# Optimization experiments

Hardware: AMD Instinct MI355X
Metric: run time of the kernel (lower is better)

Reference implementation:

```python
import jax, jax.numpy as jnp
import numpy as np

IMAGE_W, IMAGE_H = 1024, 800
STRIDES = (8, 16, 32, 64, 128)
LEVEL_HW = ((100, 128), (50, 64), (25, 32), (13, 16), (7, 8))
TOP_N = 1000
MIN_SCORE = 0.01
NMS_THR = 0.6
MAX_DET = 100
NUM_CLASSES = 80
BATCH = 16


def _grid(h, w, stride, b):
    ys = (jnp.arange(h, dtype=jnp.float32) + 0.5) * stride
    xs = (jnp.arange(w, dtype=jnp.float32) + 0.5) * stride
    gx, gy = jnp.meshgrid(xs, ys)  # [h, w]
    pos = jnp.stack([gx, gy], axis=-1)  # [h, w, 2] = (x, y)
    return jnp.broadcast_to(pos, (b, h, w, 2))


def setup_inputs() -> dict:
    key = jax.random.key(0)
    inp = {}
    for i, ((h, w), s) in enumerate(zip(LEVEL_HW, STRIDES)):
        key, k1, k2, k3 = jax.random.split(key, 4)
        inp[f"cls{i}"] = jax.random.normal(k1, (BATCH, h, w, NUM_CLASSES), jnp.float32)
        # +3 so exp(reg) gives realistic ~20px box extents
        inp[f"reg{i}"] = jax.random.normal(k2, (BATCH, h, w, 4), jnp.float32) + 3.0
        inp[f"ctr{i}"] = jax.random.normal(k3, (BATCH, h, w, 1), jnp.float32)
        inp[f"pos{i}"] = _grid(h, w, s, BATCH)
    return inp


def _level_filter(cls, reg, ctr, pos):
    b = cls.shape[0]
    cls = jax.nn.sigmoid(cls).reshape(b, -1, NUM_CLASSES)
    reg = jnp.exp(reg).reshape(b, -1, 4)
    ctr = jax.nn.sigmoid(ctr).reshape(b, -1)
    pos = pos.reshape(b, -1, 2)
    scores = jnp.sqrt(jnp.max(cls, axis=2) * ctr)  # [b, n]
    classes = jnp.argmax(cls, axis=2)  # [b, n] int
    if scores.shape[1] >= TOP_N:
        scores, idx = jax.lax.top_k(scores, TOP_N)
        classes = jnp.take_along_axis(classes, idx, axis=1)
        reg = jnp.take_along_axis(reg, idx[..., None], axis=1)
        pos = jnp.take_along_axis(pos, idx[..., None], axis=1)
        cls = jnp.take_along_axis(cls, idx[..., None], axis=1)
    return scores, classes, reg, pos, cls


def _decode_boxes(reg, pos):
    # ltrb offsets -> x1y1x2y2, truncate to int (torch .int()), clamp to image
    xy_min = pos - reg[..., 0:2]
    xy_max = pos + reg[..., 2:4]
    bx = jnp.trunc(jnp.concatenate([xy_min, xy_max], axis=-1))
    x1 = jnp.maximum(bx[..., 0], 0.0)
    y1 = jnp.maximum(bx[..., 1], 0.0)
    x2 = jnp.minimum(bx[..., 2], IMAGE_W - 1.0)
    y2 = jnp.minimum(bx[..., 3], IMAGE_H - 1.0)
    return jnp.stack([x1, y1, x2, y2], axis=-1)


def _nms_image(scores, classes, boxes, clsp):
    valid = scores > MIN_SCORE
    order = jnp.argsort(jnp.where(valid, -scores, jnp.inf))  # valid, desc score first
    s = scores[order]
    c = classes[order].astype(jnp.float32)
    b = boxes[order]
    cp = clsp[order]
    v = valid[order]
    # pairwise IoU (keep/suppress decisions are not differentiated)
    bb = jax.lax.stop_gradient(b)
    area = (bb[:, 2] - bb[:, 0]) * (bb[:, 3] - bb[:, 1])
    lt = jnp.maximum(bb[:, None, :2], bb[None, :, :2])
    rb = jnp.minimum(bb[:, None, 2:], bb[None, :, 2:])
    wh = jnp.maximum(rb - lt, 0.0)
    inter = wh[..., 0] * wh[..., 1]
    iou = inter / (area[:, None] + area[None, :] - inter)
    n = s.shape[0]
    idxs = jnp.arange(n)

    def body(i, keep):
        sup = keep[i] & (iou[i] > NMS_THR) & (idxs > i)
        return keep & ~sup

    keep = jax.lax.fori_loop(0, n, body, v)
    rank = jnp.cumsum(keep) - 1
    slot = jnp.where(keep & (rank < MAX_DET), rank, MAX_DET)  # MAX_DET -> dropped
    out_s = jnp.full((MAX_DET,), -1.0, jnp.float32).at[slot].set(s, mode="drop")
    out_c = jnp.full((MAX_DET,), -1.0, jnp.float32).at[slot].set(c, mode="drop")
    out_b = jnp.full((MAX_DET, 4), -1.0, jnp.float32).at[slot].set(b, mode="drop")
    out_cp = jnp.full((MAX_DET, NUM_CLASSES), -1.0, jnp.float32).at[slot].set(cp, mode="drop")
    return out_s, out_c, out_b, out_cp


def reference(cls0, cls1, cls2, cls3, cls4, reg0, reg1, reg2, reg3, reg4,
              ctr0, ctr1, ctr2, ctr3, ctr4, pos0, pos1, pos2, pos3, pos4):
    clss = [cls0, cls1, cls2, cls3, cls4]
    regs = [reg0, reg1, reg2, reg3, reg4]
    ctrs = [ctr0, ctr1, ctr2, ctr3, ctr4]
    poss = [pos0, pos1, pos2, pos3, pos4]
    parts = [_level_filter(c, r, t, p) for c, r, t, p in zip(clss, regs, ctrs, poss)]
    scores = jnp.concatenate([p[0] for p in parts], axis=1)
    classes = jnp.concatenate([p[1] for p in parts], axis=1)
    reg = jnp.concatenate([p[2] for p in parts], axis=1)
    pos = jnp.concatenate([p[3] for p in parts], axis=1)
    clsp = jnp.concatenate([p[4] for p in parts], axis=1)
    boxes = _decode_boxes(reg, pos)
    return jax.vmap(_nms_image)(scores, classes, boxes, clsp)
```

## Files before the change

### kernel.cpp

```cpp
#include <hip/hip_runtime.h>
#include <math.h>

#define TOTAL_G 17064
#define BATCHN  16
#define ALLF    0xFFFFFFFFFFFFFFFFull
#define INVALID_HI 0xC3DC28F5u

typedef unsigned long long u64;
typedef unsigned int u32;
typedef unsigned short u16;

#define KEYS0_OFF   0
#define KEYS1_OFF   1638400
#define KEYS234_OFF 2048000
#define CLSI_OFF    2187264
#define NC_OFF      2733312
#define T512_OFF    2733824
#define KR_OFF      2733952
#define MSK_OFF     2799488
#define SLOTK_OFF   3323776

struct Ptrs {
  const float *cls0,*cls1,*cls2,*cls3,*cls4;
  const float *reg0,*reg1,*reg2,*reg3,*reg4;
  const float *ctr0,*ctr1,*ctr2,*ctr3,*ctr4;
  const float *pos0,*pos1,*pos2,*pos3,*pos4;
  char *ws;
};

__device__ __forceinline__ float sigd(float x) {
  return (float)(1.0 / (1.0 + exp(-(double)x)));
}
__device__ __forceinline__ float dexp(float x) {
  return (float)exp((double)x);
}
__device__ __forceinline__ void levinfo(int gid, int& lev, int& idx, int& nl) {
  if      (gid < 12800) { lev=0; idx=gid;        nl=12800; }
  else if (gid < 16000) { lev=1; idx=gid-12800;  nl=3200;  }
  else if (gid < 16800) { lev=2; idx=gid-16000;  nl=800;   }
  else if (gid < 17008) { lev=3; idx=gid-16800;  nl=208;   }
  else                  { lev=4; idx=gid-17008;  nl=56;    }
}

__device__ __forceinline__ u64* krank_of(char* ws, int b) {
  return (u64*)(ws + KR_OFF + (size_t)b * 4096);
}
__device__ __forceinline__ u64* msk_of(char* ws, int b) {
  return (u64*)(ws + MSK_OFF + (size_t)b * 32768);
}
__device__ __forceinline__ u64* slotkey_of(char* ws, int b) {
  return (u64*)(ws + SLOTK_OFF + (size_t)b * 800);
}

__device__ __forceinline__ float4 decode_box(const Ptrs& P, int b, int gid) {
  int lev, idx, nl; levinfo(gid, lev, idx, nl);
  const float *rp, *pp;
  if      (lev == 0) { rp = P.reg0; pp = P.pos0; }
  else if (lev == 1) { rp = P.reg1; pp = P.pos1; }
  else if (lev == 2) { rp = P.reg2; pp = P.pos2; }
  else if (lev == 3) { rp = P.reg3; pp = P.pos3; }
  else               { rp = P.reg4; pp = P.pos4; }
  float4 rv = *(const float4*)(rp + (size_t)(b * nl + idx) * 4);
  float2 pv = *(const float2*)(pp + (size_t)(b * nl + idx) * 2);
  float e0 = dexp(rv.x), e1 = dexp(rv.y), e2 = dexp(rv.z), e3 = dexp(rv.w);
  float x1 = truncf(pv.x - e0), y1 = truncf(pv.y - e1);
  float x2 = truncf(pv.x + e2), y2 = truncf(pv.y + e3);
  x1 = fmaxf(x1, 0.0f); y1 = fmaxf(y1, 0.0f);
  x2 = fminf(x2, 1023.0f); y2 = fminf(y2, 799.0f);
  return make_float4(x1, y1, x2, y2);
}

__global__ __launch_bounds__(256) void k_score(Ptrs P) {
  __shared__ float4 sk4[64 * 20];
  int b = blockIdx.y;
  int tid = threadIdx.x;
  int p0 = blockIdx.x * 64;

  #pragma unroll
  for (int it = 0; it < 5; ++it) {
    int t4 = it * 256 + tid;
    int g = p0 + t4 / 20;
    if (g < TOTAL_G) {
      int sub = t4 - (t4 / 20) * 20;
      int lev, idx, nl; levinfo(g, lev, idx, nl);
      const float* clsb;
      if      (lev == 0) clsb = P.cls0;
      else if (lev == 1) clsb = P.cls1;
      else if (lev == 2) clsb = P.cls2;
      else if (lev == 3) clsb = P.cls3;
      else               clsb = P.cls4;
      sk4[t4] = ((const float4*)(clsb + (size_t)(b * nl + idx) * 80))[sub];
    }
  }
  __syncthreads();

  int lp = tid >> 2, q = tid & 3;
  int g = p0 + lp;
  if (g >= TOTAL_G) return;

  const float4* my4 = &sk4[lp * 20 + q * 5];
  float m = -INFINITY, m2 = -INFINITY; int mi = 0;
  #pragma unroll
  for (int k = 0; k < 5; ++k) {
    float4 v = my4[k];
    int base = q * 20 + 4 * k;
    if (v.x > m) { m2 = m; m = v.x; mi = base+0; } else if (v.x > m2) m2 = v.x;
    if (v.y > m) { m2 = m; m = v.y; mi = base+1; } else if (v.y > m2) m2 = v.y;
    if (v.z > m) { m2 = m; m = v.z; mi = base+2; } else if (v.z > m2) m2 = v.z;
    if (v.w > m) { m2 = m; m = v.w; mi = base+3; } else if (v.w > m2) m2 = v.w;
  }
  #pragma unroll
  for (int xw = 1; xw <= 2; xw <<= 1) {
    float om  = __shfl_xor(m,  xw);
    float om2 = __shfl_xor(m2, xw);
    int   omi = __shfl_xor(mi, xw);
    bool take = (om > m) || (om == m && omi < mi);
    float lm  = take ? m : om;
    float wm2 = take ? om2 : m2;
    if (take) { m = om; mi = omi; }
    m2 = fmaxf(lm, wm2);
  }

  float thr = fminf(m - 1e-3f, 9.0f);
  float pmax; int ci;
  if (m2 >= thr) {
    float pv = -1.0f; int pi = 0x7fffffff;
    #pragma unroll 1
    for (int k = 0; k < 5; ++k) {
      float4 v = my4[k];
      float xs[4] = {v.x, v.y, v.z, v.w};
      #pragma unroll
      for (int e = 0; e < 4; ++e) {
        if (xs[e] >= thr) {
          float p = sigd(xs[e]);
          if (p > pv) { pv = p; pi = q * 20 + 4 * k + e; }
        }
      }
    }
    #pragma unroll
    for (int xw = 1; xw <= 2; xw <<= 1) {
      float ov = __shfl_xor(pv, xw);
      int   oi = __shfl_xor(pi, xw);
      if (ov > pv || (ov == pv && oi < pi)) { pv = ov; pi = oi; }
    }
    pmax = pv; ci = pi;
  } else {
    pmax = sigd(m); ci = mi;
  }

  if (q == 0) {
    int lev, idx, nl; levinfo(g, lev, idx, nl);
    const float* ctrb;
    if      (lev == 0) ctrb = P.ctr0;
    else if (lev == 1) ctrb = P.ctr1;
    else if (lev == 2) ctrb = P.ctr2;
    else if (lev == 3) ctrb = P.ctr3;
    else               ctrb = P.ctr4;
    float tc = ctrb[(size_t)b * nl + idx];
    float csig = sigd(tc);
    float prod = pmax * csig;
    float s = (float)sqrt((double)prod);
    ((u16*)(P.ws + CLSI_OFF))[(size_t)b * TOTAL_G + g] = (u16)ci;
    unsigned hi = ~__float_as_uint(s);
    u64 key = ((u64)hi << 15) | (unsigned)g;
    if      (lev == 0) ((u64*)(P.ws + KEYS0_OFF))  [(size_t)b * 12800 + idx] = key;
    else if (lev == 1) ((u64*)(P.ws + KEYS1_OFF))  [(size_t)b * 3200  + idx] = key;
    else               ((u64*)(P.ws + KEYS234_OFF))[(size_t)b * 1088  + (g - 16000)] = key;
  }
}

__device__ __forceinline__ u64 loadkey(const Ptrs& P, int b, int u) {
  if (u < 12800) return ((const u64*)(P.ws + KEYS0_OFF))  [(size_t)b * 12800 + u];
  if (u < 16000) return ((const u64*)(P.ws + KEYS1_OFF))  [(size_t)b * 3200  + (u - 12800)];
  return               ((const u64*)(P.ws + KEYS234_OFF))[(size_t)b * 1088  + (u - 16000)];
}
__device__ __forceinline__ ulonglong2 loadkey2(const Ptrs& P, int b, int u) {
  if (u < 12800) return *(const ulonglong2*)((const u64*)(P.ws + KEYS0_OFF)   + (size_t)b * 12800 + u);
  if (u < 16000) return *(const ulonglong2*)((const u64*)(P.ws + KEYS1_OFF)   + (size_t)b * 3200  + (u - 12800));
  return               *(const ulonglong2*)((const u64*)(P.ws + KEYS234_OFF) + (size_t)b * 1088  + (u - 16000));
}
__device__ __forceinline__ bool keep_pred(u64 k, int u, u64 T0, u64 T1) {
  bool valid = (u32)(k >> 15) < INVALID_HI;
  bool sel = (u < 12800) ? (k <= T0) : ((u < 16000) ? (k <= T1) : true);
  return valid && sel;
}

__global__ __launch_bounds__(1024) void k_mask(Ptrs P) {
  __shared__ union USh {
    u32 H[4][4096];
    struct { float4 sbox[512]; u64 smaskR[4096]; u16 parts[1024]; } M;
  } U;
  __shared__ u64 skey[512];
  __shared__ u16 srank[512];
  __shared__ int wbase[144];
  __shared__ int sN5;
  __shared__ u64 sBoundary;
  int qi = blockIdx.x, b = blockIdx.y;
  int tid = threadIdx.x, wid = tid >> 6, lane = tid & 63;
  int rep = wid & 3;
  char* ws = P.ws;

  ulonglong2 kk[9];
  #pragma unroll
  for (int it = 0; it < 9; ++it) kk[it] = loadkey2(P, b, it * 2048 + tid * 2);

  for (int i = tid; i < 4 * 4096; i += 1024) (&U.H[0][0])[i] = 0;
  __syncthreads();
  #pragma unroll
  for (int it = 0; it < 9; ++it) {
    int u = it * 2048 + tid * 2;
    if (u < TOTAL_G && (u32)(kk[it].x >> 15) < INVALID_HI)
      atomicAdd(&U.H[rep][(u32)(kk[it].x >> 29) & 0xFFF], 1u);
    if (u + 1 < TOTAL_G && (u32)(kk[it].y >> 15) < INVALID_HI)
      atomicAdd(&U.H[rep][(u32)(kk[it].y >> 29) & 0xFFF], 1u);
  }
  __syncthreads();
  for (int i = tid; i < 4096; i += 1024)
    U.H[0][i] = U.H[0][i] + U.H[1][i] + U.H[2][i] + U.H[3][i];
  __syncthreads();

  if (wid == 0) {
    u32 ssum = 0;
    #pragma unroll 8
    for (int i = 0; i < 64; ++i) {
      int ii = (i + lane) & 63;
      ssum += U.H[0][(lane << 6) + ii];
    }
    u32 inc = ssum;
    for (int o = 1; o < 64; o <<= 1) { u32 v = __shfl_up(inc, o); if (lane >= o) inc += v; }
    u64 ball = __ballot(inc >= 512u);
    if (!ball) {
      if (lane == 0) sBoundary = ((u64)INVALID_HI << 15);
    } else {
      int Wq = __ffsll(ball) - 1;
      u32 cumBefore = __shfl(inc - ssum, Wq);
      u32 v2 = U.H[0][(Wq << 6) + lane];
      u32 inc2 = v2;
      for (int o = 1; o < 64; o <<= 1) { u32 x = __shfl_up(inc2, o); if (lane >= o) inc2 += x; }
      u64 ball2 = __ballot(cumBefore + inc2 >= 512u);
      int l2 = __ffsll(ball2) - 1;
      if (lane == 0) {
        int d = (Wq << 6) + l2;
        sBoundary = (48ull << 41) | ((u64)d << 29);
      }
    }
  }
  __syncthreads();
  u64 Boundary = sBoundary;
  if (qi == 0 && tid == 0) ((u64*)(ws + T512_OFF))[b] = Boundary - 1;

  #pragma unroll
  for (int it = 0; it < 9; ++it) {
    int u = it * 2048 + tid * 2;
    bool k0 = (u     < TOTAL_G) && ((u32)(kk[it].x >> 15) < INVALID_HI) && (kk[it].x < Boundary);
    bool k1 = (u + 1 < TOTAL_G) && ((u32)(kk[it].y >> 15) < INVALID_HI) && (kk[it].y < Boundary);
    u64 b0 = __ballot(k0), b1 = __ballot(k1);
    if (lane == 0) wbase[it * 16 + wid] = __popcll(b0) + __popcll(b1);
  }
  __syncthreads();
  if (wid == 0) {
    int carry = 0;
    for (int base = 0; base < 144; base += 64) {
      int idx = base + lane;
      int v = (idx < 144) ? wbase[idx] : 0;
      int inc = v;
      for (int o = 1; o < 64; o <<= 1) { int x = __shfl_up(inc, o); if (lane >= o) inc += x; }
      if (idx < 144) wbase[idx] = inc - v + carry;
      carry += __shfl(inc, 63);
    }
    if (lane == 0) sN5 = carry;
  }
  __syncthreads();
  int n512 = sN5;
  if (qi == 0 && tid == 0) ((int*)(ws + NC_OFF))[16 + b] = n512;

  #pragma unroll
  for (int it = 0; it < 9; ++it) {
    int u = it * 2048 + tid * 2;
    bool k0 = (u     < TOTAL_G) && ((u32)(kk[it].x >> 15) < INVALID_HI) && (kk[it].x < Boundary);
    bool k1 = (u + 1 < TOTAL_G) && ((u32)(kk[it].y >> 15) < INVALID_HI) && (kk[it].y < Boundary);
    u64 b0 = __ballot(k0), b1 = __ballot(k1);
    u64 lm = (1ull << lane) - 1ull;
    int pos0 = wbase[it * 16 + wid] + __popcll(b0 & lm) + __popcll(b1 & lm);
    int pos1 = pos0 + (k0 ? 1 : 0);
    if (k0) skey[pos0] = kk[it].x;
    if (k1) skey[pos1] = kk[it].y;
  }
  __syncthreads();

  if (tid < 512) {
    if (tid < n512) {
      U.M.sbox[tid] = decode_box(P, b, (int)(skey[tid] & 0x7FFF));
    } else {
      skey[tid] = (ALLF - 511) + (u64)tid;
      U.M.sbox[tid] = make_float4(-1e30f, -1e30f, -1e30f, -1e30f);
    }
  }
  for (int i = tid; i < 512 * 8; i += 1024) U.M.smaskR[i] = 0ull;
  __syncthreads();

  {
    int t2 = tid & 511, half = tid >> 9;
    u64 mykey = skey[t2];
    int jb = half << 8, cnt = 0;
    #pragma unroll 4
    for (int j = jb; j < jb + 256; ++j) cnt += (skey[j] < mykey) ? 1 : 0;
    U.M.parts[tid] = (u16)cnt;
  }
  __syncthreads();
  if (tid < 512) srank[tid] = (u16)(U.M.parts[tid] + U.M.parts[tid + 512]);
  __syncthreads();

  int i = qi * 128 + (tid >> 3);
  int w = tid & 7;
  float4 bi = U.M.sbox[i];
  u64 ki = skey[i];
  int ri = srank[i];
  float ia = (bi.z - bi.x) * (bi.w - bi.y);
  #pragma unroll 8
  for (int bj = 0; bj < 64; ++bj) {
    int jj = (bj + w) & 63;
    int j = (w << 6) | jj;
    u64 kj = skey[j];
    if (ki < kj) {
      float4 bj4 = U.M.sbox[j];
      float ja  = (bj4.z - bj4.x) * (bj4.w - bj4.y);
      float ltx = fmaxf(bi.x, bj4.x), lty = fmaxf(bi.y, bj4.y);
      float rbx = fminf(bi.z, bj4.z), rby = fminf(bi.w, bj4.w);
      float wv = fmaxf(rbx - ltx, 0.0f), hv = fmaxf(rby - lty, 0.0f);
      float inter = wv * hv;
      float iou = inter / (ia + ja - inter);
      if (iou > 0.6f) {
        int rj = srank[j];
        atomicOr(&U.M.smaskR[ri * 8 + (rj >> 6)], 1ull << (rj & 63));
      }
    }
  }
  __syncthreads();

  {
    int il = tid >> 3, ww = tid & 7;
    int ig = qi * 128 + il;
    if (ig < n512) {
      int r = srank[ig];
      msk_of(ws, b)[r * 8 + ww] = U.M.smaskR[r * 8 + ww];
      if (ww == 0) krank_of(ws, b)[r] = skey[ig];
    }
  }
}

__device__ u64 select256(const u64* keys, int n, int t0, u32* hist, u64* shP, int* shT) {
  u64 Pfx = 3; int t = t0;
  const int SS[4] = {33, 21, 9, 0};
  const int WW[4] = {12, 12, 12, 9};
  for (int p = 0; p < 4; ++p) {
    int s = SS[p], wb = WW[p];
    u32 dmask = (1u << wb) - 1u;
    for (int i = threadIdx.x; i < 4096; i += 256) hist[i] = 0;
    __syncthreads();
    for (int i = threadIdx.x; i < n; i += 256) {
      u64 k = keys[i];
      if ((k >> (s + wb)) == Pfx) atomicAdd(&hist[(u32)(k >> s) & dmask], 1u);
    }
    __syncthreads();
    if (threadIdx.x < 64) {
      int lane = threadIdx.x;
      u32 ssum = 0;
      for (int i = 0; i < 64; ++i) ssum += hist[(lane << 6) + ((i + lane) & 63)];
      u32 inc = ssum;
      for (int o = 1; o < 64; o <<= 1) { u32 v = __shfl_up(inc, o); if (lane >= o) inc += v; }
      u64 ball = __ballot(inc >= (u32)t);
      int Wq = __ffsll(ball) - 1;
      u32 cumBefore = __shfl(inc - ssum, Wq);
      u32 v2 = hist[(Wq << 6) + lane];
      u32 inc2 = v2;
      for (int o = 1; o < 64; o <<= 1) { u32 x = __shfl_up(inc2, o); if (lane >= o) inc2 += x; }
      u64 ball2 = __ballot(cumBefore + inc2 >= (u32)t);
      int l2 = __ffsll(ball2) - 1;
      u32 cumB2 = __shfl(cumBefore + inc2 - v2, l2);
      if (lane == 0) { *shP = (Pfx << wb) | (u32)((Wq << 6) + l2); *shT = t - (int)cumB2; }
    }
    __syncthreads();
    Pfx = *shP; t = *shT;
    __syncthreads();
  }
  return Pfx;
}

__global__ __launch_bounds__(256) void k_reduce(Ptrs P) {
  __shared__ u64 smask[4096];
  __shared__ u32 keeplist[100];
  __shared__ int keptS;
  __shared__ u64 liveC[267];
  __shared__ union UF {
    u32 hist[4096];
    struct { u64 pk[256]; int pc[256]; float4 fkb[100]; } F;
  } UF_;
  __shared__ u64 shP; __shared__ int shT;
  __shared__ u64 bk; __shared__ int bc2;

  int b = blockIdx.x;
  int tid = threadIdx.x;
  char* ws = P.ws;
  int n512 = ((int*)(ws + NC_OFF))[16 + b];
  const u64* kr = krank_of(ws, b);

  const u64* gmask = msk_of(ws, b);
  for (int t = tid; t < 4096; t += 256) smask[t] = gmask[t];
  __syncthreads();

  if (tid < 64) {
    int lane = tid;
    u64 lw = 0;
    if (lane < 8) {
      int lo = lane << 6;
      int c = n512 - lo; if (c < 0) c = 0; if (c > 64) c = 64;
      lw = (c >= 64) ? ALLF : ((c > 0) ? ((1ull << c) - 1ull) : 0ull);
    }
    int kept = 0;
    while (kept < 100) {
      bool nz = (lane < 8) && (lw != 0ull);
      u64 bal = __ballot(nz);
      if (!bal) break;
      int W = __ffsll(bal) - 1;
      u64 wv = __shfl(lw, W);
      int bit = __ffsll(wv) - 1;
      int i = (W << 6) + bit;
      if (lane == 0) keeplist[kept] = (u32)i;
      kept++;
      if (lane == W) lw &= ~(1ull << bit);
      if (kept == 100) break;
      if (lane < 8) lw &= ~smask[i * 8 + lane];
    }
    if (lane == 0) keptS = kept;
  }
  __syncthreads();
  int kept = keptS;
  int keptW = kept;

  if (kept < 100) {
    u64 T0 = select256((const u64*)(ws + KEYS0_OFF) + (size_t)b * 12800, 12800, 1000,
                       UF_.hist, &shP, &shT);
    u64 T1 = select256((const u64*)(ws + KEYS1_OFF) + (size_t)b * 3200, 3200, 1000,
                       UF_.hist, &shP, &shT);
    u64 T512 = ((u64*)(ws + T512_OFF))[b];
    for (int w = tid; w < 267; w += 256) {
      int lo = w << 6;
      u64 m = 0;
      for (int e = 0; e < 64; ++e) {
        int u = lo + e;
        if (u < TOTAL_G) {
          u64 k = loadkey(P, b, u);
          if (keep_pred(k, u, T0, T1) && k > T512) m |= (1ull << e);
        }
      }
      liveC[w] = m;
    }
    if (tid < kept) UF_.F.fkb[tid] = decode_box(P, b, (int)(kr[keeplist[tid]] & 0x7FFF));
    __syncthreads();

    for (int k2 = 0; k2 < kept; ++k2) {
      float4 bi = UF_.F.fkb[k2];
      float ia = (bi.z - bi.x) * (bi.w - bi.y);
      for (int u = tid; u < TOTAL_G; u += 256) {
        if (!((liveC[u >> 6] >> (u & 63)) & 1ull)) continue;
        float4 bj4 = decode_box(P, b, u);
        float ja  = (bj4.z - bj4.x) * (bj4.w - bj4.y);
        float ltx = fmaxf(bi.x, bj4.x), lty = fmaxf(bi.y, bj4.y);
        float rbx = fminf(bi.z, bj4.z), rby = fminf(bi.w, bj4.w);
        float wv = fmaxf(rbx - ltx, 0.0f), hv = fmaxf(rby - lty, 0.0f);
        float inter = wv * hv;
        float iou = inter / (ia + ja - inter);
        if (iou > 0.6f) atomicAnd(&liveC[u >> 6], ~(1ull << (u & 63)));
      }
    }
    __syncthreads();

    while (kept < 100) {
      u64 mymin = ALLF; int myc = -1;
      for (int u = tid; u < TOTAL_G; u += 256) {
        if (!((liveC[u >> 6] >> (u & 63)) & 1ull)) continue;
        u64 k = loadkey(P, b, u);
        if (k < mymin) { mymin = k; myc = u; }
      }
      UF_.F.pk[tid] = mymin; UF_.F.pc[tid] = myc;
      __syncthreads();
      if (tid < 64) {
        u64 m = UF_.F.pk[tid]; int c0 = UF_.F.pc[tid];
        #pragma unroll
        for (int o = 64; o < 256; o += 64)
          if (UF_.F.pk[tid + o] < m) { m = UF_.F.pk[tid + o]; c0 = UF_.F.pc[tid + o]; }
        for (int o = 32; o > 0; o >>= 1) {
          u64 om = __shfl_down(m, o); int oc = __shfl_down(c0, o);
          if (om < m) { m = om; c0 = oc; }
        }
        if (tid == 0) { bk = m; bc2 = c0; }
      }
      __syncthreads();
      if (bk == ALLF) break;
      int cs = bc2;
      if (tid == 0) {
        slotkey_of(ws, b)[kept] = bk;
        atomicAnd(&liveC[cs >> 6], ~(1ull << (cs & 63)));
      }
      __syncthreads();
      kept++;
      if (kept == 100) break;
      float4 bi = decode_box(P, b, cs);
      float ia = (bi.z - bi.x) * (bi.w - bi.y);
      for (int u = tid; u < TOTAL_G; u += 256) {
        if (!((liveC[u >> 6] >> (u & 63)) & 1ull)) continue;
        float4 bj4 = decode_box(P, b, u);
        float ja  = (bj4.z - bj4.x) * (bj4.w - bj4.y);
        float ltx = fmaxf(bi.x, bj4.x), lty = fmaxf(bi.y, bj4.y);
        float rbx = fminf(bi.z, bj4.z), rby = fminf(bi.w, bj4.w);
        float wv = fmaxf(rbx - ltx, 0.0f), hv = fmaxf(rby - lty, 0.0f);
        float inter = wv * hv;
        float iou = inter / (ia + ja - inter);
        if (iou > 0.6f) atomicAnd(&liveC[u >> 6], ~(1ull << (u & 63)));
      }
      __syncthreads();
    }
  }

  if (tid < 100) {
    if (tid < keptW)      slotkey_of(ws, b)[tid] = kr[keeplist[tid]];
    else if (tid >= kept) slotkey_of(ws, b)[tid] = ALLF;
  }
}

__global__ __launch_bounds__(256) void k_out(Ptrs P, float* out) {
  int b = blockIdx.x, part = blockIdx.y;
  int s0 = part * 10;
  int tid = threadIdx.x;
  const u64* skl = slotkey_of(P.ws, b);

  if (tid < 10) {
    int s = s0 + tid;
    u64 key = skl[s];
    float os = -1.0f, oc = -1.0f;
    float4 bx = make_float4(-1.0f, -1.0f, -1.0f, -1.0f);
    if (key != ALLF) {
      int gid = (int)(key & 0x7FFF);
      os = __uint_as_float(~(u32)(key >> 15));
      oc = (float)((u16*)(P.ws + CLSI_OFF))[(size_t)b * TOTAL_G + gid];
      bx = decode_box(P, b, gid);
    }
    out[b * 100 + s] = os;
    out[1600 + b * 100 + s] = oc;
    *(float4*)(out + 3200 + (size_t)(b * 100 + s) * 4) = bx;
  }

  for (int t = tid; t < 800; t += 256) {
    int sl = t / 80, k = t - sl * 80;
    int s = s0 + sl;
    u64 key = skl[s];
    float val = -1.0f;
    if (key != ALLF) {
      int gid = (int)(key & 0x7FFF);
      int lev, idx, nl; levinfo(gid, lev, idx, nl);
      const float* cp;
      if      (lev == 0) cp = P.cls0;
      else if (lev == 1) cp = P.cls1;
      else if (lev == 2) cp = P.cls2;
      else if (lev == 3) cp = P.cls3;
      else               cp = P.cls4;
      val = sigd(cp[(size_t)(b * nl + idx) * 80 + k]);
    }
    out[9600 + (size_t)(b * 100 + s) * 80 + k] = val;
  }
}

extern "C" void kernel_launch(void* const* d_in, const int* in_sizes, int n_in,
                              void* d_out, int out_size, void* d_ws, size_t ws_size,
                              hipStream_t stream) {
  (void)in_sizes; (void)n_in; (void)out_size; (void)ws_size;
  Ptrs P;
  P.cls0 = (const float*)d_in[0];  P.reg0 = (const float*)d_in[1];
  P.ctr0 = (const float*)d_in[2];  P.pos0 = (const float*)d_in[3];
  P.cls1 = (const float*)d_in[4];  P.reg1 = (const float*)d_in[5];
  P.ctr1 = (const float*)d_in[6];  P.pos1 = (const float*)d_in[7];
  P.cls2 = (const float*)d_in[8];  P.reg2 = (const float*)d_in[9];
  P.ctr2 = (const float*)d_in[10]; P.pos2 = (const float*)d_in[11];
  P.cls3 = (const float*)d_in[12]; P.reg3 = (const float*)d_in[13];
  P.ctr3 = (const float*)d_in[14]; P.pos3 = (const float*)d_in[15];
  P.cls4 = (const float*)d_in[16]; P.reg4 = (const float*)d_in[17];
  P.ctr4 = (const float*)d_in[18]; P.pos4 = (const float*)d_in[19];
  P.ws = (char*)d_ws;

  k_score<<<dim3(267, 16), 256, 0, stream>>>(P);
  k_mask<<<dim3(4, 16), 1024, 0, stream>>>(P);
  k_reduce<<<16, 256, 0, stream>>>(P);
  k_out<<<dim3(16, 10), 256, 0, stream>>>(P, (float*)d_out);
}
```

Before: 91.41 us.

## Fuse mask, reduce and output kernels via last-block-done atomic counter

Merges the mask-building, greedy NMS reduction and output-writing kernels into one launch. The last of the four blocks per image, found with an atomic counter plus threadfence, runs the serial reduction and writes outputs directly, keeping slot keys and the boundary threshold in shared memory instead of the workspace. The reduction now runs with 1024 threads instead of 256. This removes two kernel launches and their global round trips, but the output writing is now done by only 16 blocks instead of 160, and the larger shared union may lower occupancy.

```diff
diff --git a/kernel.cpp b/kernel.cpp
--- a/kernel.cpp
+++ b/kernel.cpp
@@ -15,10 +15,8 @@
 #define KEYS234_OFF 2048000
 #define CLSI_OFF    2187264
 #define NC_OFF      2733312
-#define T512_OFF    2733824
 #define KR_OFF      2733952
 #define MSK_OFF     2799488
-#define SLOTK_OFF   3323776
 
 struct Ptrs {
   const float *cls0,*cls1,*cls2,*cls3,*cls4;
@@ -47,9 +45,6 @@
 }
 __device__ __forceinline__ u64* msk_of(char* ws, int b) {
   return (u64*)(ws + MSK_OFF + (size_t)b * 32768);
-}
-__device__ __forceinline__ u64* slotkey_of(char* ws, int b) {
-  return (u64*)(ws + SLOTK_OFF + (size_t)b * 800);
 }
 
 __device__ __forceinline__ float4 decode_box(const Ptrs& P, int b, int gid) {
@@ -75,6 +70,8 @@
   int b = blockIdx.y;
   int tid = threadIdx.x;
   int p0 = blockIdx.x * 64;
+
+  if (blockIdx.x == 0 && tid == 0) ((int*)(P.ws + NC_OFF))[b] = 0;
 
   #pragma unroll
   for (int it = 0; it < 5; ++it) {
@@ -185,16 +182,63 @@
   return valid && sel;
 }
 
-__global__ __launch_bounds__(1024) void k_mask(Ptrs P) {
+__device__ u64 select1024(const u64* keys, int n, int t0, u32* hist, u64* shP, int* shT) {
+  u64 Pfx = 3; int t = t0;
+  const int SS[4] = {33, 21, 9, 0};
+  const int WW[4] = {12, 12, 12, 9};
+  for (int p = 0; p < 4; ++p) {
+    int s = SS[p], wb = WW[p];
+    u32 dmask = (1u << wb) - 1u;
+    for (int i = threadIdx.x; i < 4096; i += 1024) hist[i] = 0;
+    __syncthreads();
+    for (int i = threadIdx.x; i < n; i += 1024) {
+      u64 k = keys[i];
+      if ((k >> (s + wb)) == Pfx) atomicAdd(&hist[(u32)(k >> s) & dmask], 1u);
+    }
+    __syncthreads();
+    if (threadIdx.x < 64) {
+      int lane = threadIdx.x;
+      u32 ssum = 0;
+      for (int i = 0; i < 64; ++i) ssum += hist[(lane << 6) + ((i + lane) & 63)];
+      u32 inc = ssum;
+      for (int o = 1; o < 64; o <<= 1) { u32 v = __shfl_up(inc, o); if (lane >= o) inc += v; }
+      u64 ball = __ballot(inc >= (u32)t);
+      int Wq = __ffsll(ball) - 1;
+      u32 cumBefore = __shfl(inc - ssum, Wq);
+      u32 v2 = hist[(Wq << 6) + lane];
+      u32 inc2 = v2;
+      for (int o = 1; o < 64; o <<= 1) { u32 x = __shfl_up(inc2, o); if (lane >= o) inc2 += x; }
+      u64 ball2 = __ballot(cumBefore + inc2 >= (u32)t);
+      int l2 = __ffsll(ball2) - 1;
+      u32 cumB2 = __shfl(cumBefore + inc2 - v2, l2);
+      if (lane == 0) { *shP = (Pfx << wb) | (u32)((Wq << 6) + l2); *shT = t - (int)cumB2; }
+    }
+    __syncthreads();
+    Pfx = *shP; t = *shT;
+    __syncthreads();
+  }
+  return Pfx;
+}
+
+__global__ __launch_bounds__(1024) void k_maskred(Ptrs P, float* out) {
   __shared__ union USh {
     u32 H[4][4096];
     struct { float4 sbox[512]; u64 smaskR[4096]; u16 parts[1024]; } M;
+    struct { u64 smask[4096]; u32 hist[4096]; u64 pk[1024]; int pc[1024];
+             float4 fkb[100]; } R;
   } U;
   __shared__ u64 skey[512];
   __shared__ u16 srank[512];
   __shared__ int wbase[144];
   __shared__ int sN5;
   __shared__ u64 sBoundary;
+  __shared__ int sLast;
+  __shared__ u64 skl[100];
+  __shared__ u32 keeplist[100];
+  __shared__ int keptS;
+  __shared__ u64 liveC[267];
+  __shared__ u64 shP; __shared__ int shT;
+  __shared__ u64 bkS; __shared__ int bc2S;
   int qi = blockIdx.x, b = blockIdx.y;
   int tid = threadIdx.x, wid = tid >> 6, lane = tid & 63;
   int rep = wid & 3;
@@ -247,7 +291,6 @@
   }
   __syncthreads();
   u64 Boundary = sBoundary;
-  if (qi == 0 && tid == 0) ((u64*)(ws + T512_OFF))[b] = Boundary - 1;
 
   #pragma unroll
   for (int it = 0; it < 9; ++it) {
@@ -272,7 +315,6 @@
   }
   __syncthreads();
   int n512 = sN5;
-  if (qi == 0 && tid == 0) ((int*)(ws + NC_OFF))[16 + b] = n512;
 
   #pragma unroll
   for (int it = 0; it < 9; ++it) {
@@ -311,28 +353,30 @@
   if (tid < 512) srank[tid] = (u16)(U.M.parts[tid] + U.M.parts[tid + 512]);
   __syncthreads();
 
-  int i = qi * 128 + (tid >> 3);
-  int w = tid & 7;
-  float4 bi = U.M.sbox[i];
-  u64 ki = skey[i];
-  int ri = srank[i];
-  float ia = (bi.z - bi.x) * (bi.w - bi.y);
-  #pragma unroll 8
-  for (int bj = 0; bj < 64; ++bj) {
-    int jj = (bj + w) & 63;
-    int j = (w << 6) | jj;
-    u64 kj = skey[j];
-    if (ki < kj) {
-      float4 bj4 = U.M.sbox[j];
-      float ja  = (bj4.z - bj4.x) * (bj4.w - bj4.y);
-      float ltx = fmaxf(bi.x, bj4.x), lty = fmaxf(bi.y, bj4.y);
-      float rbx = fminf(bi.z, bj4.z), rby = fminf(bi.w, bj4.w);
-      float wv = fmaxf(rbx - ltx, 0.0f), hv = fmaxf(rby - lty, 0.0f);
-      float inter = wv * hv;
-      float iou = inter / (ia + ja - inter);
-      if (iou > 0.6f) {
-        int rj = srank[j];
-        atomicOr(&U.M.smaskR[ri * 8 + (rj >> 6)], 1ull << (rj & 63));
+  {
+    int i = qi * 128 + (tid >> 3);
+    int w = tid & 7;
+    float4 bi = U.M.sbox[i];
+    u64 ki = skey[i];
+    int ri = srank[i];
+    float ia = (bi.z - bi.x) * (bi.w - bi.y);
+    #pragma unroll 8
+    for (int bj = 0; bj < 64; ++bj) {
+      int jj = (bj + w) & 63;
+      int j = (w << 6) | jj;
+      u64 kj = skey[j];
+      if (ki < kj) {
+        float4 bj4 = U.M.sbox[j];
+        float ja  = (bj4.z - bj4.x) * (bj4.w - bj4.y);
+        float ltx = fmaxf(bi.x, bj4.x), lty = fmaxf(bi.y, bj4.y);
+        float rbx = fminf(bi.z, bj4.z), rby = fminf(bi.w, bj4.w);
+        float wv = fmaxf(rbx - ltx, 0.0f), hv = fmaxf(rby - lty, 0.0f);
+        float inter = wv * hv;
+        float iou = inter / (ia + ja - inter);
+        if (iou > 0.6f) {
+          int rj = srank[j];
+          atomicOr(&U.M.smaskR[ri * 8 + (rj >> 6)], 1ull << (rj & 63));
+        }
       }
     }
   }
@@ -347,104 +391,60 @@
       if (ww == 0) krank_of(ws, b)[r] = skey[ig];
     }
   }
-}
-
-__device__ u64 select256(const u64* keys, int n, int t0, u32* hist, u64* shP, int* shT) {
-  u64 Pfx = 3; int t = t0;
-  const int SS[4] = {33, 21, 9, 0};
-  const int WW[4] = {12, 12, 12, 9};
-  for (int p = 0; p < 4; ++p) {
-    int s = SS[p], wb = WW[p];
-    u32 dmask = (1u << wb) - 1u;
-    for (int i = threadIdx.x; i < 4096; i += 256) hist[i] = 0;
-    __syncthreads();
-    for (int i = threadIdx.x; i < n; i += 256) {
-      u64 k = keys[i];
-      if ((k >> (s + wb)) == Pfx) atomicAdd(&hist[(u32)(k >> s) & dmask], 1u);
-    }
-    __syncthreads();
-    if (threadIdx.x < 64) {
-      int lane = threadIdx.x;
-      u32 ssum = 0;
-      for (int i = 0; i < 64; ++i) ssum += hist[(lane << 6) + ((i + lane) & 63)];
-      u32 inc = ssum;
-      for (int o = 1; o < 64; o <<= 1) { u32 v = __shfl_up(inc, o); if (lane >= o) inc += v; }
-      u64 ball = __ballot(inc >= (u32)t);
-      int Wq = __ffsll(ball) - 1;
-      u32 cumBefore = __shfl(inc - ssum, Wq);
-      u32 v2 = hist[(Wq << 6) + lane];
-      u32 inc2 = v2;
-      for (int o = 1; o < 64; o <<= 1) { u32 x = __shfl_up(inc2, o); if (lane >= o) inc2 += x; }
-      u64 ball2 = __ballot(cumBefore + inc2 >= (u32)t);
-      int l2 = __ffsll(ball2) - 1;
-      u32 cumB2 = __shfl(cumBefore + inc2 - v2, l2);
-      if (lane == 0) { *shP = (Pfx << wb) | (u32)((Wq << 6) + l2); *shT = t - (int)cumB2; }
-    }
-    __syncthreads();
-    Pfx = *shP; t = *shT;
-    __syncthreads();
-  }
-  return Pfx;
-}
-
-__global__ __launch_bounds__(256) void k_reduce(Ptrs P) {
-  __shared__ u64 smask[4096];
-  __shared__ u32 keeplist[100];
-  __shared__ int keptS;
-  __shared__ u64 liveC[267];
-  __shared__ union UF {
-    u32 hist[4096];
-    struct { u64 pk[256]; int pc[256]; float4 fkb[100]; } F;
-  } UF_;
-  __shared__ u64 shP; __shared__ int shT;
-  __shared__ u64 bk; __shared__ int bc2;
-
-  int b = blockIdx.x;
-  int tid = threadIdx.x;
-  char* ws = P.ws;
-  int n512 = ((int*)(ws + NC_OFF))[16 + b];
+  __threadfence();
+  __syncthreads();
+  if (tid == 0) {
+    int old = atomicAdd(&((int*)(ws + NC_OFF))[b], 1);
+    sLast = (old == 3);
+  }
+  __syncthreads();
+  if (!sLast) return;
+  __threadfence();
+
   const u64* kr = krank_of(ws, b);
-
   const u64* gmask = msk_of(ws, b);
-  for (int t = tid; t < 4096; t += 256) smask[t] = gmask[t];
+  for (int t = tid; t < 4096; t += 1024) U.R.smask[t] = gmask[t];
   __syncthreads();
 
   if (tid < 64) {
-    int lane = tid;
+    int lane2 = tid;
     u64 lw = 0;
-    if (lane < 8) {
-      int lo = lane << 6;
+    if (lane2 < 8) {
+      int lo = lane2 << 6;
       int c = n512 - lo; if (c < 0) c = 0; if (c > 64) c = 64;
       lw = (c >= 64) ? ALLF : ((c > 0) ? ((1ull << c) - 1ull) : 0ull);
     }
     int kept = 0;
     while (kept < 100) {
-      bool nz = (lane < 8) && (lw != 0ull);
+      bool nz = (lane2 < 8) && (lw != 0ull);
       u64 bal = __ballot(nz);
       if (!bal) break;
       int W = __ffsll(bal) - 1;
       u64 wv = __shfl(lw, W);
       int bit = __ffsll(wv) - 1;
       int i = (W << 6) + bit;
-      if (lane == 0) keeplist[kept] = (u32)i;
+      if (lane2 == 0) keeplist[kept] = (u32)i;
       kept++;
-      if (lane == W) lw &= ~(1ull << bit);
+      if (lane2 == W) lw &= ~(1ull << bit);
       if (kept == 100) break;
-      if (lane < 8) lw &= ~smask[i * 8 + lane];
-    }
-    if (lane == 0) keptS = kept;
+      if (lane2 < 8) lw &= ~U.R.smask[i * 8 + lane2];
+    }
+    if (lane2 == 0) keptS = kept;
   }
   __syncthreads();
   int kept = keptS;
   int keptW = kept;
 
+  if (tid < 100) skl[tid] = (tid < keptW) ? kr[keeplist[tid]] : ALLF;
+  __syncthreads();
+
   if (kept < 100) {
-    u64 T0 = select256((const u64*)(ws + KEYS0_OFF) + (size_t)b * 12800, 12800, 1000,
-                       UF_.hist, &shP, &shT);
-    u64 T1 = select256((const u64*)(ws + KEYS1_OFF) + (size_t)b * 3200, 3200, 1000,
-                       UF_.hist, &shP, &shT);
-    u64 T512 = ((u64*)(ws + T512_OFF))[b];
-    for (int w = tid; w < 267; w += 256) {
+    u64 T0 = select1024((const u64*)(ws + KEYS0_OFF) + (size_t)b * 12800, 12800, 1000,
+                        U.R.hist, &shP, &shT);
+    u64 T1 = select1024((const u64*)(ws + KEYS1_OFF) + (size_t)b * 3200, 3200, 1000,
+                        U.R.hist, &shP, &shT);
+    u64 T512 = Boundary - 1;
+    for (int w = tid; w < 267; w += 1024) {
       int lo = w << 6;
       u64 m = 0;
       for (int e = 0; e < 64; ++e) {
@@ -456,13 +456,13 @@
       }
       liveC[w] = m;
     }
-    if (tid < kept) UF_.F.fkb[tid] = decode_box(P, b, (int)(kr[keeplist[tid]] & 0x7FFF));
+    if (tid < kept) U.R.fkb[tid] = decode_box(P, b, (int)(kr[keeplist[tid]] & 0x7FFF));
     __syncthreads();
 
     for (int k2 = 0; k2 < kept; ++k2) {
-      float4 bi = UF_.F.fkb[k2];
+      float4 bi = U.R.fkb[k2];
       float ia = (bi.z - bi.x) * (bi.w - bi.y);
-      for (int u = tid; u < TOTAL_G; u += 256) {
+      for (int u = tid; u < TOTAL_G; u += 1024) {
         if (!((liveC[u >> 6] >> (u & 63)) & 1ull)) continue;
         float4 bj4 = decode_box(P, b, u);
         float ja  = (bj4.z - bj4.x) * (bj4.w - bj4.y);
@@ -478,29 +478,28 @@
 
     while (kept < 100) {
       u64 mymin = ALLF; int myc = -1;
-      for (int u = tid; u < TOTAL_G; u += 256) {
+      for (int u = tid; u < TOTAL_G; u += 1024) {
         if (!((liveC[u >> 6] >> (u & 63)) & 1ull)) continue;
         u64 k = loadkey(P, b, u);
         if (k < mymin) { mymin = k; myc = u; }
       }
-      UF_.F.pk[tid] = mymin; UF_.F.pc[tid] = myc;
+      U.R.pk[tid] = mymin; U.R.pc[tid] = myc;
       __syncthreads();
       if (tid < 64) {
-        u64 m = UF_.F.pk[tid]; int c0 = UF_.F.pc[tid];
-        #pragma unroll
-        for (int o = 64; o < 256; o += 64)
-          if (UF_.F.pk[tid + o] < m) { m = UF_.F.pk[tid + o]; c0 = UF_.F.pc[tid + o]; }
+        u64 m = U.R.pk[tid]; int c0 = U.R.pc[tid];
+        for (int o = 64; o < 1024; o += 64)
+          if (U.R.pk[tid + o] < m) { m = U.R.pk[tid + o]; c0 = U.R.pc[tid + o]; }
         for (int o = 32; o > 0; o >>= 1) {
           u64 om = __shfl_down(m, o); int oc = __shfl_down(c0, o);
           if (om < m) { m = om; c0 = oc; }
         }
-        if (tid == 0) { bk = m; bc2 = c0; }
+        if (tid == 0) { bkS = m; bc2S = c0; }
       }
       __syncthreads();
-      if (bk == ALLF) break;
-      int cs = bc2;
+      if (bkS == ALLF) break;
+      int cs = bc2S;
       if (tid == 0) {
-        slotkey_of(ws, b)[kept] = bk;
+        skl[kept] = bkS;
         atomicAnd(&liveC[cs >> 6], ~(1ull << (cs & 63)));
       }
       __syncthreads();
@@ -508,7 +507,7 @@
       if (kept == 100) break;
       float4 bi = decode_box(P, b, cs);
       float ia = (bi.z - bi.x) * (bi.w - bi.y);
-      for (int u = tid; u < TOTAL_G; u += 256) {
+      for (int u = tid; u < TOTAL_G; u += 1024) {
         if (!((liveC[u >> 6] >> (u & 63)) & 1ull)) continue;
         float4 bj4 = decode_box(P, b, u);
         float ja  = (bj4.z - bj4.x) * (bj4.w - bj4.y);
@@ -521,39 +520,26 @@
       }
       __syncthreads();
     }
+    __syncthreads();
   }
 
   if (tid < 100) {
-    if (tid < keptW)      slotkey_of(ws, b)[tid] = kr[keeplist[tid]];
-    else if (tid >= kept) slotkey_of(ws, b)[tid] = ALLF;
-  }
-}
-
-__global__ __launch_bounds__(256) void k_out(Ptrs P, float* out) {
-  int b = blockIdx.x, part = blockIdx.y;
-  int s0 = part * 10;
-  int tid = threadIdx.x;
-  const u64* skl = slotkey_of(P.ws, b);
-
-  if (tid < 10) {
-    int s = s0 + tid;
+    int s = tid;
     u64 key = skl[s];
     float os = -1.0f, oc = -1.0f;
     float4 bx = make_float4(-1.0f, -1.0f, -1.0f, -1.0f);
     if (key != ALLF) {
       int gid = (int)(key & 0x7FFF);
       os = __uint_as_float(~(u32)(key >> 15));
-      oc = (float)((u16*)(P.ws + CLSI_OFF))[(size_t)b * TOTAL_G + gid];
+      oc = (float)((u16*)(ws + CLSI_OFF))[(size_t)b * TOTAL_G + gid];
       bx = decode_box(P, b, gid);
     }
     out[b * 100 + s] = os;
     out[1600 + b * 100 + s] = oc;
     *(float4*)(out + 3200 + (size_t)(b * 100 + s) * 4) = bx;
   }
-
-  for (int t = tid; t < 800; t += 256) {
-    int sl = t / 80, k = t - sl * 80;
-    int s = s0 + sl;
+  for (int t = tid; t < 100 * 80; t += 1024) {
+    int s = t / 80, k = t - s * 80;
     u64 key = skl[s];
     float val = -1.0f;
     if (key != ALLF) {
@@ -589,7 +575,5 @@
   P.ws = (char*)d_ws;
 
   k_score<<<dim3(267, 16), 256, 0, stream>>>(P);
-  k_mask<<<dim3(4, 16), 1024, 0, stream>>>(P);
-  k_reduce<<<16, 256, 0, stream>>>(P);
-  k_out<<<dim3(16, 10), 256, 0, stream>>>(P, (float*)d_out);
-}
+  k_maskred<<<dim3(4, 16), 1024, 0, stream>>>(P, (float*)d_out);
+}
```

Result: slower. 125.2 us (+37.0%).
